# Optimization experiments

Measured on AMD Instinct MI355X. Metric: run time of the kernel, lower is better.

Reference implementation:

```python
import jax, jax.numpy as jnp
import numpy as np

B, T, D, P, M = 4, 1024, 512, 64, 256


def setup_inputs() -> dict:
    key = jax.random.key(0)
    ks = jax.random.split(key, 10)
    s_d = 1.0 / np.sqrt(D)
    s_m = 1.0 / np.sqrt(M)
    s_p = 1.0 / np.sqrt(P)
    return {
        "inputs": jax.random.normal(ks[0], (B, T, D), dtype=jnp.float32),
        "ec": jax.random.normal(ks[1], (B, M), dtype=jnp.float32),
        "W1": jax.random.uniform(ks[2], (D, P), jnp.float32, -s_d, s_d),
        "b1": jax.random.uniform(ks[3], (P,), jnp.float32, -s_d, s_d),
        "W2": jax.random.uniform(ks[4], (D, P), jnp.float32, -s_d, s_d),
        "b2": jax.random.uniform(ks[5], (P,), jnp.float32, -s_d, s_d),
        "W3": jax.random.uniform(ks[6], (M, P), jnp.float32, -s_m, s_m),
        "b3": jax.random.uniform(ks[7], (P,), jnp.float32, -s_m, s_m),
        "wa_w": jax.random.uniform(ks[8], (P,), jnp.float32, -s_p, s_p),
        "wa_b": jax.random.uniform(ks[9], (), jnp.float32, -s_p, s_p),
    }


def reference(inputs, ec, W1, b1, W2, b2, W3, b3, wa_w, wa_b):
    # inputs: (B,T,D), ec: (B,M)
    w1h = inputs @ W1 + b1          # (B,T,P)
    w2h = inputs @ W2 + b2          # (B,T,P)
    w3e = ec @ W3 + b3              # (B,P)
    # Gt: (B,T,T,P) via broadcast add + tanh
    gt = jnp.tanh(w1h[:, :, None, :] + w2h[:, None, :, :] + w3e[:, None, None, :])
    at = jnp.einsum('btup,p->btu', gt, wa_w) + wa_b   # (B,T,T)
    at = jax.nn.softmax(at, axis=-1)
    out = jnp.einsum('btu,bud->btd', at, inputs)      # (B,T,D)
    return out
```

## Files before the change

kernel.cpp:

```cpp
#include <hip/hip_runtime.h>
#include <hip/hip_bf16.h>

constexpr int BB = 4;
constexpr int TT = 1024;
constexpr int DD = 512;
constexpr int PP = 64;
constexpr int MM = 256;

constexpr float CSCALE = 2.8853900817779268f;
constexpr float L2E = 1.4426950408889634f;

typedef __attribute__((ext_vector_type(8))) short v8s;
typedef __attribute__((ext_vector_type(4))) float v4f;
typedef unsigned int __attribute__((address_space(1))) gu32;
typedef unsigned int __attribute__((address_space(3))) su32;

__device__ __forceinline__ unsigned short f2bf(float f) {
    unsigned u = __builtin_bit_cast(unsigned, f);
    unsigned r = (u + 0x7fffu + ((u >> 16) & 1u)) >> 16;
    return (unsigned short)r;
}
__device__ __forceinline__ float bf2f(unsigned short h) {
    return __builtin_bit_cast(float, (unsigned)h << 16);
}
__device__ __forceinline__ void split2(float v, unsigned short& h, unsigned short& l) {
    unsigned short hh = f2bf(v);
    h = hh;
    l = f2bf(v - bf2f(hh));
}
__device__ __forceinline__ void gld_lds16(const void* g, void* l) {
    __builtin_amdgcn_global_load_lds((const gu32*)g, (su32*)l, 16, 0, 0);
}

__global__ __launch_bounds__(256) void prep1_kernel(
    const float* __restrict__ x, const float* __restrict__ ec,
    const float* __restrict__ W1, const float* __restrict__ W2,
    const float* __restrict__ W3, const float* __restrict__ b3,
    unsigned short* __restrict__ xt,
    unsigned short* __restrict__ WhT, unsigned short* __restrict__ WlT,
    float* __restrict__ E3) {
    __shared__ float tile[64][65];
    int bid = blockIdx.x;
    int tid = threadIdx.x;
    if (bid < 512) {
        int d0 = (bid & 7) << 6;
        int u0 = ((bid >> 3) & 15) << 6;
        int b = bid >> 7;
        int c4 = (tid & 15) << 2, r = tid >> 4;
        #pragma unroll
        for (int i = 0; i < 4; i++) {
            int row = r + (i << 4);
            float4 v = *(const float4*)(x + ((size_t)b * TT + u0 + row) * DD + d0 + c4);
            tile[row][c4 + 0] = v.x;
            tile[row][c4 + 1] = v.y;
            tile[row][c4 + 2] = v.z;
            tile[row][c4 + 3] = v.w;
        }
        __syncthreads();
        int dd = tid >> 2;
        int uq = (tid & 3) << 4;
        unsigned short us[16];
        #pragma unroll
        for (int j = 0; j < 16; j++) us[j] = f2bf(tile[uq + j][dd]);
        uint4 w0, w1;
        w0.x = us[0] | ((unsigned)us[1] << 16);  w0.y = us[2] | ((unsigned)us[3] << 16);
        w0.z = us[4] | ((unsigned)us[5] << 16);  w0.w = us[6] | ((unsigned)us[7] << 16);
        w1.x = us[8] | ((unsigned)us[9] << 16);  w1.y = us[10] | ((unsigned)us[11] << 16);
        w1.z = us[12] | ((unsigned)us[13] << 16); w1.w = us[14] | ((unsigned)us[15] << 16);
        unsigned short* dst = xt + ((size_t)b * DD + d0 + dd) * TT + u0 + uq;
        *(uint4*)dst = w0;
        *(uint4*)(dst + 8) = w1;
    } else if (bid < 528) {
        int w = bid - 512;
        int n = tid >> 1;
        int kb = (w << 5) + ((tid & 1) << 4);
        unsigned short hs[16], ls[16];
        #pragma unroll
        for (int kk = 0; kk < 16; kk++) {
            int k = kb + kk;
            float v = (n < 64) ? W1[k * PP + n] : W2[k * PP + (n - 64)];
            split2(v, hs[kk], ls[kk]);
        }
        uint4 a, bqq;
        a.x = hs[0] | ((unsigned)hs[1] << 16);   a.y = hs[2] | ((unsigned)hs[3] << 16);
        a.z = hs[4] | ((unsigned)hs[5] << 16);   a.w = hs[6] | ((unsigned)hs[7] << 16);
        bqq.x = hs[8] | ((unsigned)hs[9] << 16); bqq.y = hs[10] | ((unsigned)hs[11] << 16);
        bqq.z = hs[12] | ((unsigned)hs[13] << 16); bqq.w = hs[14] | ((unsigned)hs[15] << 16);
        *(uint4*)(WhT + (size_t)n * DD + kb) = a;
        *(uint4*)(WhT + (size_t)n * DD + kb + 8) = bqq;
        a.x = ls[0] | ((unsigned)ls[1] << 16);   a.y = ls[2] | ((unsigned)ls[3] << 16);
        a.z = ls[4] | ((unsigned)ls[5] << 16);   a.w = ls[6] | ((unsigned)ls[7] << 16);
        bqq.x = ls[8] | ((unsigned)ls[9] << 16); bqq.y = ls[10] | ((unsigned)ls[11] << 16);
        bqq.z = ls[12] | ((unsigned)ls[13] << 16); bqq.w = ls[14] | ((unsigned)ls[15] << 16);
        *(uint4*)(WlT + (size_t)n * DD + kb) = a;
        *(uint4*)(WlT + (size_t)n * DD + kb + 8) = bqq;
    } else {
        int b = tid >> 6, p = tid & 63;
        float a = b3[p];
        const float* e = ec + (size_t)b * MM;
        #pragma unroll 4
        for (int m = 0; m < MM; m++) a = fmaf(e[m], W3[m * PP + p], a);
        E3[b * PP + p] = __builtin_amdgcn_exp2f(a * CSCALE);
    }
}

__global__ __launch_bounds__(256) void prep2_kernel(
    const float* __restrict__ x,
    const unsigned short* __restrict__ WhT, const unsigned short* __restrict__ WlT,
    const float* __restrict__ b1, const float* __restrict__ b2,
    float* __restrict__ E1, float* __restrict__ E2) {
    __shared__ unsigned short AsH[16][72];
    __shared__ unsigned short AsL[16][72];
    __shared__ unsigned short BsH[128][72];
    __shared__ unsigned short BsL[128][72];
    int m0 = blockIdx.x << 4;
    int tid = threadIdx.x;
    int lane = tid & 63;
    int wv = tid >> 6;
    int wn = wv << 5;
    int l15 = lane & 15;
    int quad = lane >> 4;

    v4f acc[2];
    acc[0] = (v4f){0.f, 0.f, 0.f, 0.f};
    acc[1] = acc[0];

    for (int k0 = 0; k0 < DD; k0 += 64) {
        __syncthreads();
        {
            int row = tid >> 4, k4 = (tid & 15) << 2;
            float4 v = *(const float4*)(x + (size_t)(m0 + row) * DD + k0 + k4);
            unsigned short h0, h1, h2, h3, l0, l1, l2, l3;
            split2(v.x, h0, l0); split2(v.y, h1, l1);
            split2(v.z, h2, l2); split2(v.w, h3, l3);
            uint2 hw, lw;
            hw.x = h0 | ((unsigned)h1 << 16); hw.y = h2 | ((unsigned)h3 << 16);
            lw.x = l0 | ((unsigned)l1 << 16); lw.y = l2 | ((unsigned)l3 << 16);
            *(uint2*)&AsH[row][k4] = hw;
            *(uint2*)&AsL[row][k4] = lw;
        }
        #pragma unroll
        for (int i = 0; i < 4; i++) {
            int s = (i << 8) + tid;
            int row = s >> 3, k8 = (s & 7) << 3;
            *(uint4*)&BsH[row][k8] = *(const uint4*)(WhT + (size_t)row * DD + k0 + k8);
            *(uint4*)&BsL[row][k8] = *(const uint4*)(WlT + (size_t)row * DD + k0 + k8);
        }
        __syncthreads();
        #pragma unroll
        for (int kk = 0; kk < 64; kk += 32) {
            int kc = kk + (quad << 3);
            v8s aH0 = *(const v8s*)&AsH[l15][kc];
            v8s aL0 = *(const v8s*)&AsL[l15][kc];
            #pragma unroll
            for (int nt = 0; nt < 2; nt++) {
                v8s bH = *(const v8s*)&BsH[wn + (nt << 4) + l15][kc];
                v8s bL = *(const v8s*)&BsL[wn + (nt << 4) + l15][kc];
                acc[nt] = __builtin_amdgcn_mfma_f32_16x16x32_bf16(aH0, bH, acc[nt], 0, 0, 0);
                acc[nt] = __builtin_amdgcn_mfma_f32_16x16x32_bf16(aH0, bL, acc[nt], 0, 0, 0);
                acc[nt] = __builtin_amdgcn_mfma_f32_16x16x32_bf16(aL0, bH, acc[nt], 0, 0, 0);
            }
        }
    }
    #pragma unroll
    for (int nt = 0; nt < 2; nt++) {
        int n = wn + (nt << 4) + l15;
        int p = n & 63;
        float bias = (n < 64) ? b1[p] : b2[p];
        float* E = (n < 64) ? E1 : E2;
        int rbase = m0 + (quad << 2);
        #pragma unroll
        for (int r = 0; r < 4; r++) {
            float h = acc[nt][r] + bias;
            E[(size_t)(rbase + r) * PP + p] = __builtin_amdgcn_exp2f(h * CSCALE);
        }
    }
}

__global__ __launch_bounds__(256) void scores_kernel(
    const float* __restrict__ E1, const float* __restrict__ E2,
    const float* __restrict__ E3, const float* __restrict__ wa_w,
    const float* __restrict__ wa_b, unsigned short* __restrict__ at_bf) {
    __shared__ float sm[4][4];
    __shared__ float sl[4][4];
    int tid = threadIdx.x;
    int bid = blockIdx.x;
    int b = bid >> 8;
    int t0 = (bid & 255) << 2;
    int pp = tid & 7;
    int uu = tid >> 3;
    int p0 = pp << 3;
    int lane = tid & 63;
    int wv = tid >> 6;
    int my_i = pp & 3;
    bool pbit1 = (pp & 2) != 0;
    bool pbit0 = (pp & 1) != 0;

    float ww2[8], H[4][8];
    float base;
    {
        float4 wv0 = *(const float4*)(wa_w + p0);
        float4 wv1 = *(const float4*)(wa_w + p0 + 4);
        float s = wv0.x + wv0.y + wv0.z + wv0.w + wv1.x + wv1.y + wv1.z + wv1.w;
        s += __shfl_xor(s, 1, 64);
        s += __shfl_xor(s, 2, 64);
        s += __shfl_xor(s, 4, 64);
        base = (s + wa_b[0]) * L2E;
        ww2[0] = -2.f * L2E * wv0.x; ww2[1] = -2.f * L2E * wv0.y;
        ww2[2] = -2.f * L2E * wv0.z; ww2[3] = -2.f * L2E * wv0.w;
        ww2[4] = -2.f * L2E * wv1.x; ww2[5] = -2.f * L2E * wv1.y;
        ww2[6] = -2.f * L2E * wv1.z; ww2[7] = -2.f * L2E * wv1.w;
        float4 e3a = *(const float4*)(E3 + (b << 6) + p0);
        float4 e3b = *(const float4*)(E3 + (b << 6) + p0 + 4);
        #pragma unroll
        for (int i = 0; i < 4; i++) {
            const float* e1p = E1 + (((size_t)(b << 10) + t0 + i) << 6) + p0;
            float4 a = *(const float4*)e1p;
            float4 c = *(const float4*)(e1p + 4);
            H[i][0] = a.x * e3a.x; H[i][1] = a.y * e3a.y; H[i][2] = a.z * e3a.z; H[i][3] = a.w * e3a.w;
            H[i][4] = c.x * e3b.x; H[i][5] = c.y * e3b.y; H[i][6] = c.z * e3b.z; H[i][7] = c.w * e3b.w;
        }
    }

    float own[32];
    float mown = -1e30f;
    #pragma unroll
    for (int k = 0; k < 32; k++) {
        int u = (k << 5) + uu;
        const float* ep = E2 + (((size_t)(b << 10) + u) << 6) + p0;
        float4 e0 = *(const float4*)ep;
        float4 e1 = *(const float4*)(ep + 4);
        float ev[8] = {e0.x, e0.y, e0.z, e0.w, e1.x, e1.y, e1.z, e1.w};
        float s0 = 0.f, s1 = 0.f, s2 = 0.f, s3 = 0.f;
        #pragma unroll
        for (int j = 0; j < 8; j++) {
            s0 = fmaf(ww2[j], __builtin_amdgcn_rcpf(fmaf(H[0][j], ev[j], 1.0f)), s0);
            s1 = fmaf(ww2[j], __builtin_amdgcn_rcpf(fmaf(H[1][j], ev[j], 1.0f)), s1);
            s2 = fmaf(ww2[j], __builtin_amdgcn_rcpf(fmaf(H[2][j], ev[j], 1.0f)), s2);
            s3 = fmaf(ww2[j], __builtin_amdgcn_rcpf(fmaf(H[3][j], ev[j], 1.0f)), s3);
        }
        s0 += __shfl_xor(s0, 4, 64);
        s1 += __shfl_xor(s1, 4, 64);
        s2 += __shfl_xor(s2, 4, 64);
        s3 += __shfl_xor(s3, 4, 64);
        float op0 = pbit1 ? s2 : s0;
        float op1 = pbit1 ? s3 : s1;
        float ot0 = pbit1 ? s0 : s2;
        float ot1 = pbit1 ? s1 : s3;
        op0 += __shfl_xor(ot0, 2, 64);
        op1 += __shfl_xor(ot1, 2, 64);
        float osel = pbit0 ? op1 : op0;
        float osnd = pbit0 ? op0 : op1;
        osel += __shfl_xor(osnd, 1, 64);
        float o = osel + base;
        own[k] = o;
        mown = fmaxf(mown, o);
    }
    mown = fmaxf(mown, __shfl_xor(mown, 8, 64));
    mown = fmaxf(mown, __shfl_xor(mown, 16, 64));
    mown = fmaxf(mown, __shfl_xor(mown, 32, 64));
    if (lane < 4) sm[wv][lane] = mown;
    __syncthreads();
    float mx = fmaxf(fmaxf(sm[0][my_i], sm[1][my_i]), fmaxf(sm[2][my_i], sm[3][my_i]));

    float l = 0.f;
    #pragma unroll
    for (int k = 0; k < 32; k++) {
        float e = __builtin_amdgcn_exp2f(own[k] - mx);
        own[k] = e;
        l += e;
    }
    l += __shfl_xor(l, 8, 64);
    l += __shfl_xor(l, 16, 64);
    l += __shfl_xor(l, 32, 64);
    if (lane < 4) sl[wv][lane] = l;
    __syncthreads();
    float inv = 1.0f / (sl[0][my_i] + sl[1][my_i] + sl[2][my_i] + sl[3][my_i]);

    if (pp < 4) {
        size_t rowbase = ((size_t)((b << 10) + t0 + my_i)) << 10;
        #pragma unroll
        for (int k = 0; k < 32; k++) {
            at_bf[rowbase + (k << 5) + uu] = f2bf(own[k] * inv);
        }
    }
}

__global__ __launch_bounds__(256) void av_mfma_kernel(
    const unsigned short* __restrict__ at_bf, const unsigned short* __restrict__ xt,
    float* __restrict__ out) {
    __shared__ unsigned short As[64 * 64];
    __shared__ unsigned short Bs[64 * 64];
    int b = blockIdx.z;
    int m0 = blockIdx.y << 6;
    int n0 = blockIdx.x << 6;
    const unsigned short* A = at_bf + ((size_t)b << 20);
    const unsigned short* Bt = xt + (size_t)b * DD * TT;
    int tid = threadIdx.x;
    int lane = tid & 63;
    int wv = tid >> 6;
    int wm = (wv & 1) << 5;
    int wn = (wv >> 1) << 5;
    int l15 = lane & 15;
    int quad = lane >> 4;

    int sr = lane >> 3;
    int scg = (lane & 7) ^ sr;

    v4f acc00 = {0.f, 0.f, 0.f, 0.f}, acc01 = acc00, acc10 = acc00, acc11 = acc00;

    for (int k0 = 0; k0 < TT; k0 += 64) {
        __syncthreads();
        #pragma unroll
        for (int t = 0; t < 2; t++) {
            int r0 = (wv << 4) + (t << 3);
            int row = r0 + sr;
            gld_lds16(A + (size_t)(m0 + row) * TT + k0 + (scg << 3), &As[r0 << 6]);
            gld_lds16(Bt + (size_t)(n0 + row) * TT + k0 + (scg << 3), &Bs[r0 << 6]);
        }
        __syncthreads();
        #pragma unroll
        for (int kq = 0; kq < 2; kq++) {
            int c = (kq << 2) + quad;
            int swz = (c ^ (l15 & 7)) << 3;
            v8s a0 = *(const v8s*)&As[((wm + l15) << 6) + swz];
            v8s a1 = *(const v8s*)&As[((wm + 16 + l15) << 6) + swz];
            v8s b0 = *(const v8s*)&Bs[((wn + l15) << 6) + swz];
            v8s b1 = *(const v8s*)&Bs[((wn + 16 + l15) << 6) + swz];
            acc00 = __builtin_amdgcn_mfma_f32_16x16x32_bf16(a0, b0, acc00, 0, 0, 0);
            acc01 = __builtin_amdgcn_mfma_f32_16x16x32_bf16(a0, b1, acc01, 0, 0, 0);
            acc10 = __builtin_amdgcn_mfma_f32_16x16x32_bf16(a1, b0, acc10, 0, 0, 0);
            acc11 = __builtin_amdgcn_mfma_f32_16x16x32_bf16(a1, b1, acc11, 0, 0, 0);
        }
    }
    float* C = out + (size_t)b * TT * DD;
    int rbase = m0 + wm + (quad << 2);
    int cn = n0 + wn + l15;
    #pragma unroll
    for (int r = 0; r < 4; r++) {
        C[(size_t)(rbase + r) * DD + cn]           = acc00[r];
        C[(size_t)(rbase + r) * DD + cn + 16]      = acc01[r];
        C[(size_t)(rbase + 16 + r) * DD + cn]      = acc10[r];
        C[(size_t)(rbase + 16 + r) * DD + cn + 16] = acc11[r];
    }
}

extern "C" void kernel_launch(void* const* d_in, const int* in_sizes, int n_in,
                              void* d_out, int out_size, void* d_ws, size_t ws_size,
                              hipStream_t stream) {
    const float* inputs = (const float*)d_in[0];
    const float* ec     = (const float*)d_in[1];
    const float* W1     = (const float*)d_in[2];
    const float* b1     = (const float*)d_in[3];
    const float* W2     = (const float*)d_in[4];
    const float* b2     = (const float*)d_in[5];
    const float* W3     = (const float*)d_in[6];
    const float* b3     = (const float*)d_in[7];
    const float* wa_w   = (const float*)d_in[8];
    const float* wa_b   = (const float*)d_in[9];
    float* out = (float*)d_out;

    float* ws = (float*)d_ws;
    float* E1 = ws;
    float* E2 = ws + 262144;
    float* E3 = ws + 524288;
    unsigned short* at_bf = (unsigned short*)(ws + 524800);
    unsigned short* xt    = (unsigned short*)(ws + 524800 + 2097152);
    unsigned short* WhT   = at_bf;
    unsigned short* WlT   = at_bf + 65536;

    hipLaunchKernelGGL(prep1_kernel, dim3(529), dim3(256), 0, stream,
                       inputs, ec, W1, W2, W3, b3, xt, WhT, WlT, E3);
    hipLaunchKernelGGL(prep2_kernel, dim3(256), dim3(256), 0, stream,
                       inputs, WhT, WlT, b1, b2, E1, E2);
    hipLaunchKernelGGL(scores_kernel, dim3(1024), dim3(256), 0, stream,
                       E1, E2, E3, wa_w, wa_b, at_bf);
    hipLaunchKernelGGL(av_mfma_kernel, dim3(DD / 64, TT / 64, BB), dim3(256), 0, stream,
                       at_bf, xt, out);
}
```

Before: 157.5 us.

## Combine reciprocal sums into single fraction with packed FP32 FMA

Rewrites the per-u score computation so that the eight reciprocal terms sum_j w_j/d_j are merged into one numerator/denominator pair through a pairwise fraction-combining tree. Only one rcp is then issued per output instead of eight. The arithmetic runs on two-wide float vectors so the compiler can emit packed FP32 FMA/MUL instructions that handle two t rows at once. This trades transcendental-unit throughput for extra multiplies. It risks overflow or precision loss from forming products of eight denominators.

```diff
diff --git a/kernel.cpp b/kernel.cpp
--- a/kernel.cpp
+++ b/kernel.cpp
@@ -12,6 +12,7 @@
 
 typedef __attribute__((ext_vector_type(8))) short v8s;
 typedef __attribute__((ext_vector_type(4))) float v4f;
+typedef __attribute__((ext_vector_type(2))) float v2f;
 typedef unsigned int __attribute__((address_space(1))) gu32;
 typedef unsigned int __attribute__((address_space(3))) su32;
 
@@ -30,6 +31,9 @@
 }
 __device__ __forceinline__ void gld_lds16(const void* g, void* l) {
     __builtin_amdgcn_global_load_lds((const gu32*)g, (su32*)l, 16, 0, 0);
+}
+__device__ __forceinline__ v2f pfma(v2f a, v2f b, v2f c) {
+    return __builtin_elementwise_fma(a, b, c);
 }
 
 __global__ __launch_bounds__(256) void prep1_kernel(
@@ -196,7 +200,8 @@
     bool pbit1 = (pp & 2) != 0;
     bool pbit0 = (pp & 1) != 0;
 
-    float ww2[8], H[4][8];
+    v2f ww2p[8];
+    v2f Hp[2][8];
     float base;
     {
         float4 wv0 = *(const float4*)(wa_w + p0);
@@ -206,12 +211,16 @@
         s += __shfl_xor(s, 2, 64);
         s += __shfl_xor(s, 4, 64);
         base = (s + wa_b[0]) * L2E;
+        float ww2[8];
         ww2[0] = -2.f * L2E * wv0.x; ww2[1] = -2.f * L2E * wv0.y;
         ww2[2] = -2.f * L2E * wv0.z; ww2[3] = -2.f * L2E * wv0.w;
         ww2[4] = -2.f * L2E * wv1.x; ww2[5] = -2.f * L2E * wv1.y;
         ww2[6] = -2.f * L2E * wv1.z; ww2[7] = -2.f * L2E * wv1.w;
+        #pragma unroll
+        for (int j = 0; j < 8; j++) ww2p[j] = (v2f){ww2[j], ww2[j]};
         float4 e3a = *(const float4*)(E3 + (b << 6) + p0);
         float4 e3b = *(const float4*)(E3 + (b << 6) + p0 + 4);
+        float H[4][8];
         #pragma unroll
         for (int i = 0; i < 4; i++) {
             const float* e1p = E1 + (((size_t)(b << 10) + t0 + i) << 6) + p0;
@@ -220,7 +229,13 @@
             H[i][0] = a.x * e3a.x; H[i][1] = a.y * e3a.y; H[i][2] = a.z * e3a.z; H[i][3] = a.w * e3a.w;
             H[i][4] = c.x * e3b.x; H[i][5] = c.y * e3b.y; H[i][6] = c.z * e3b.z; H[i][7] = c.w * e3b.w;
         }
-    }
+        #pragma unroll
+        for (int pr = 0; pr < 2; pr++)
+            #pragma unroll
+            for (int j = 0; j < 8; j++)
+                Hp[pr][j] = (v2f){H[2 * pr][j], H[2 * pr + 1][j]};
+    }
+    const v2f one2 = (v2f){1.0f, 1.0f};
 
     float own[32];
     float mown = -1e30f;
@@ -230,15 +245,36 @@
         const float* ep = E2 + (((size_t)(b << 10) + u) << 6) + p0;
         float4 e0 = *(const float4*)ep;
         float4 e1 = *(const float4*)(ep + 4);
-        float ev[8] = {e0.x, e0.y, e0.z, e0.w, e1.x, e1.y, e1.z, e1.w};
-        float s0 = 0.f, s1 = 0.f, s2 = 0.f, s3 = 0.f;
-        #pragma unroll
-        for (int j = 0; j < 8; j++) {
-            s0 = fmaf(ww2[j], __builtin_amdgcn_rcpf(fmaf(H[0][j], ev[j], 1.0f)), s0);
-            s1 = fmaf(ww2[j], __builtin_amdgcn_rcpf(fmaf(H[1][j], ev[j], 1.0f)), s1);
-            s2 = fmaf(ww2[j], __builtin_amdgcn_rcpf(fmaf(H[2][j], ev[j], 1.0f)), s2);
-            s3 = fmaf(ww2[j], __builtin_amdgcn_rcpf(fmaf(H[3][j], ev[j], 1.0f)), s3);
-        }
+        v2f evp[8];
+        evp[0] = (v2f){e0.x, e0.x}; evp[1] = (v2f){e0.y, e0.y};
+        evp[2] = (v2f){e0.z, e0.z}; evp[3] = (v2f){e0.w, e0.w};
+        evp[4] = (v2f){e1.x, e1.x}; evp[5] = (v2f){e1.y, e1.y};
+        evp[6] = (v2f){e1.z, e1.z}; evp[7] = (v2f){e1.w, e1.w};
+        float sr_[4];
+        #pragma unroll
+        for (int pr = 0; pr < 2; pr++) {
+            v2f d0 = pfma(Hp[pr][0], evp[0], one2);
+            v2f d1 = pfma(Hp[pr][1], evp[1], one2);
+            v2f d2 = pfma(Hp[pr][2], evp[2], one2);
+            v2f d3 = pfma(Hp[pr][3], evp[3], one2);
+            v2f d4 = pfma(Hp[pr][4], evp[4], one2);
+            v2f d5 = pfma(Hp[pr][5], evp[5], one2);
+            v2f d6 = pfma(Hp[pr][6], evp[6], one2);
+            v2f d7 = pfma(Hp[pr][7], evp[7], one2);
+            v2f e01 = d0 * d1, e23 = d2 * d3, e45 = d4 * d5, e67 = d6 * d7;
+            v2f n01 = pfma(ww2p[0], d1, ww2p[1] * d0);
+            v2f n23 = pfma(ww2p[2], d3, ww2p[3] * d2);
+            v2f n45 = pfma(ww2p[4], d5, ww2p[5] * d4);
+            v2f n67 = pfma(ww2p[6], d7, ww2p[7] * d6);
+            v2f q03 = e01 * e23, q47 = e45 * e67;
+            v2f n03 = pfma(n23, e01, n01 * e23);
+            v2f n47 = pfma(n67, e45, n45 * e67);
+            v2f Dq = q03 * q47;
+            v2f Nq = pfma(n47, q03, n03 * q47);
+            sr_[2 * pr]     = Nq.x * __builtin_amdgcn_rcpf(Dq.x);
+            sr_[2 * pr + 1] = Nq.y * __builtin_amdgcn_rcpf(Dq.y);
+        }
+        float s0 = sr_[0], s1 = sr_[1], s2 = sr_[2], s3 = sr_[3];
         s0 += __shfl_xor(s0, 4, 64);
         s1 += __shfl_xor(s1, 4, 64);
         s2 += __shfl_xor(s2, 4, 64);
```

After: 149.7 us. 4.9% less time.
